# Kernel tuning notes

Hardware: AMD Instinct MI355X
Metric: run time of the kernel (lower is better)

## Reference

```python
import jax, jax.numpy as jnp
import numpy as np

D_MODEL = 512
OUT = 512
D_STATE = 16
D_CONV = 4
EXPAND = 2
N_LAYERS = 2
D_INNER = EXPAND * D_MODEL
DT_RANK = -(-D_MODEL // 16)  # ceil(d_model/16) = 32
B = 2
L = 2048


def setup_inputs() -> dict:
    key = jax.random.key(0)
    ks = jax.random.split(key, 16)
    def w(k, shape, scale):
        return jax.random.normal(k, shape, dtype=jnp.float32) * scale
    s_d = 1.0 / np.sqrt(D_MODEL)
    s_e = 1.0 / np.sqrt(D_INNER)
    s_r = 1.0 / np.sqrt(DT_RANK)
    s_f = 1.0 / np.sqrt(2 * D_MODEL)
    return {
        "x": jax.random.normal(ks[0], (B, L, D_MODEL), dtype=jnp.float32),
        "in_proj_w": w(ks[1], (N_LAYERS, 2 * D_INNER, D_MODEL), s_d),
        "conv_w": w(ks[2], (N_LAYERS, D_INNER, D_CONV), 0.5),
        "conv_b": jnp.zeros((N_LAYERS, D_INNER), jnp.float32),
        "x_proj_w": w(ks[3], (N_LAYERS, DT_RANK + 2 * D_STATE, D_INNER), s_e),
        "dt_w": w(ks[4], (N_LAYERS, D_INNER, DT_RANK), s_r),
        "dt_b": w(ks[5], (N_LAYERS, D_INNER), 0.1),
        "A_log": jnp.tile(jnp.log(jnp.arange(1, D_STATE + 1, dtype=jnp.float32))[None, None, :], (N_LAYERS, D_INNER, 1)),
        "Dp": jnp.ones((N_LAYERS, D_INNER), jnp.float32),
        "out_proj_w": w(ks[6], (N_LAYERS, D_MODEL, D_INNER), s_e),
        "rms_w": jnp.ones((N_LAYERS, D_MODEL), jnp.float32),
        "ln1_w": jnp.ones((D_MODEL,), jnp.float32),
        "ln1_b": jnp.zeros((D_MODEL,), jnp.float32),
        "ln2_w": jnp.ones((D_MODEL,), jnp.float32),
        "ln2_b": jnp.zeros((D_MODEL,), jnp.float32),
        "ffn_w1": w(ks[7], (2 * D_MODEL, D_MODEL), s_d),
        "ffn_b1": jnp.zeros((2 * D_MODEL,), jnp.float32),
        "ffn_w2": w(ks[8], (D_MODEL, 2 * D_MODEL), s_f),
        "ffn_b2": jnp.zeros((D_MODEL,), jnp.float32),
        "final_w": w(ks[9], (OUT, D_MODEL), s_d),
        "final_b": jnp.zeros((OUT,), jnp.float32),
    }


def _ln(x, w, b, eps=1e-5):
    mu = x.mean(-1, keepdims=True)
    v = ((x - mu) ** 2).mean(-1, keepdims=True)
    return (x - mu) * jax.lax.rsqrt(v + eps) * w + b


def _rms(x, w, eps=1e-5):
    return x * jax.lax.rsqrt(jnp.mean(x * x, -1, keepdims=True) + eps) * w


def _mixer(x, ipw, cw, cb, xpw, dtw, dtb, alog, dpar, opw):
    # x: [B, L, D]; single Mamba mixer (in_proj -> causal depthwise conv -> SSM -> gate -> out_proj)
    Lx = x.shape[1]
    xz = x @ ipw.T                              # [B, L, 2*ED]
    xc, z = jnp.split(xz, 2, axis=-1)
    xp = jnp.pad(xc, ((0, 0), (D_CONV - 1, 0), (0, 0)))  # causal left-pad
    xc = cb + sum(cw[:, k] * xp[:, k:k + Lx, :] for k in range(D_CONV))
    xc = jax.nn.silu(xc)
    dbc = xc @ xpw.T                            # [B, L, dt_rank + 2*N]
    delta = jax.nn.softplus(dbc[..., :DT_RANK] @ dtw.T + dtb)   # [B, L, ED]
    Bm = dbc[..., DT_RANK:DT_RANK + D_STATE]    # [B, L, N]
    Cm = dbc[..., DT_RANK + D_STATE:]           # [B, L, N]
    A = -jnp.exp(alog)                          # [ED, N]
    dA = jnp.exp(delta[..., None] * A)          # [B, L, ED, N]
    dBx = (delta * xc)[..., None] * Bm[:, :, None, :]  # [B, L, ED, N]
    def step(h, inp):
        a, bx = inp
        h = a * h + bx
        return h, h
    _, hs = jax.lax.scan(step, jnp.zeros_like(dA[:, 0]), (jnp.moveaxis(dA, 1, 0), jnp.moveaxis(dBx, 1, 0)))
    hs = jnp.moveaxis(hs, 0, 1)                 # [B, L, ED, N]
    y = jnp.einsum('blen,bln->ble', hs, Cm) + dpar * xc
    return (y * jax.nn.silu(z)) @ opw.T


def _forward(x, in_proj_w, conv_w, conv_b, x_proj_w, dt_w, dt_b, A_log, Dp, out_proj_w, rms_w,
             ln1_w, ln1_b, ln2_w, ln2_b, ffn_w1, ffn_b1, ffn_w2, ffn_b2, final_w, final_b):
    h = _ln(x, ln1_w, ln1_b)
    for i in range(N_LAYERS):  # Mamba = stack of residual RMSNorm+mixer blocks
        h = h + _mixer(_rms(h, rms_w[i]), in_proj_w[i], conv_w[i], conv_b[i], x_proj_w[i],
                       dt_w[i], dt_b[i], A_log[i], Dp[i], out_proj_w[i])
    x = x + h
    f = jax.nn.relu(_ln(x, ln2_w, ln2_b) @ ffn_w1.T + ffn_b1) @ ffn_w2.T + ffn_b2
    x = x + f
    return x @ final_w.T + final_b


def reference(x, in_proj_w, conv_w, conv_b, x_proj_w, dt_w, dt_b, A_log, Dp, out_proj_w, rms_w,
              ln1_w, ln1_b, ln2_w, ln2_b, ffn_w1, ffn_b1, ffn_w2, ffn_b2, final_w, final_b):
    return _forward(x, in_proj_w, conv_w, conv_b, x_proj_w, dt_w, dt_b, A_log, Dp, out_proj_w, rms_w,
                    ln1_w, ln1_b, ln2_w, ln2_b, ffn_w1, ffn_b1, ffn_w2, ffn_b2, final_w, final_b)
```

## Files before the change

### kernel.cpp

```cpp
#include <hip/hip_runtime.h>
#include <math.h>

#define ROWS 4096
#define LSEQ 2048
#define DM   512
#define DI   1024
#define NCH  64
#define CHT  (LSEQ / NCH)
#define NCOMB 1152

typedef __bf16 bf16_t;
typedef bf16_t bf16x8 __attribute__((ext_vector_type(8)));
typedef float f32x4 __attribute__((ext_vector_type(4)));
typedef unsigned int u32;
typedef const __attribute__((address_space(1))) u32* gp32;
typedef __attribute__((address_space(3))) u32* lp32;

__device__ __forceinline__ float siluf(float v) { return v / (1.f + expf(-v)); }
__device__ __forceinline__ float softplusf(float v) {
    return fmaxf(v, 0.f) + log1pf(expf(-fabsf(v)));
}

__global__ __launch_bounds__(256) void ln_kernel(const float* __restrict__ x,
                                                 const float* __restrict__ w,
                                                 const float* __restrict__ b,
                                                 float* __restrict__ out) {
    int row = blockIdx.x;
    int tid = threadIdx.x;
    const float* xr = x + (size_t)row * DM;
    float v0 = xr[tid], v1 = xr[tid + 256];
    float sum = v0 + v1, sq = v0 * v0 + v1 * v1;
    for (int o = 32; o > 0; o >>= 1) {
        sum += __shfl_down(sum, o);
        sq  += __shfl_down(sq, o);
    }
    __shared__ float s1[4], s2[4];
    int wid = tid >> 6, lane = tid & 63;
    if (lane == 0) { s1[wid] = sum; s2[wid] = sq; }
    __syncthreads();
    sum = s1[0] + s1[1] + s1[2] + s1[3];
    sq  = s2[0] + s2[1] + s2[2] + s2[3];
    float mu  = sum * (1.f / DM);
    float var = sq * (1.f / DM) - mu * mu;
    float r   = rsqrtf(var + 1e-5f);
    out[(size_t)row * DM + tid]       = (v0 - mu) * r * w[tid] + b[tid];
    out[(size_t)row * DM + tid + 256] = (v1 - mu) * r * w[tid + 256] + b[tid + 256];
}

__global__ __launch_bounds__(256) void ln_add_kernel(
    const float* __restrict__ x, const float* __restrict__ hres,
    const float* __restrict__ w, const float* __restrict__ b,
    float* __restrict__ x2, bf16_t* __restrict__ outb) {
    int row = blockIdx.x;
    int tid = threadIdx.x;
    size_t base = (size_t)row * DM;
    float v0 = x[base + tid] + hres[base + tid];
    float v1 = x[base + tid + 256] + hres[base + tid + 256];
    x2[base + tid] = v0;
    x2[base + tid + 256] = v1;
    float sum = v0 + v1, sq = v0 * v0 + v1 * v1;
    for (int o = 32; o > 0; o >>= 1) {
        sum += __shfl_down(sum, o);
        sq  += __shfl_down(sq, o);
    }
    __shared__ float s1[4], s2[4];
    int wid = tid >> 6, lane = tid & 63;
    if (lane == 0) { s1[wid] = sum; s2[wid] = sq; }
    __syncthreads();
    sum = s1[0] + s1[1] + s1[2] + s1[3];
    sq  = s2[0] + s2[1] + s2[2] + s2[3];
    float mu  = sum * (1.f / DM);
    float var = sq * (1.f / DM) - mu * mu;
    float r   = rsqrtf(var + 1e-5f);
    outb[base + tid]       = (bf16_t)((v0 - mu) * r * w[tid] + b[tid]);
    outb[base + tid + 256] = (bf16_t)((v1 - mu) * r * w[tid + 256] + b[tid + 256]);
}

__global__ __launch_bounds__(256) void rms_kernel(const float* __restrict__ x,
                                                  const float* __restrict__ w,
                                                  bf16_t* __restrict__ out) {
    int row = blockIdx.x;
    int tid = threadIdx.x;
    const float* xr = x + (size_t)row * DM;
    float v0 = xr[tid], v1 = xr[tid + 256];
    float sq = v0 * v0 + v1 * v1;
    for (int o = 32; o > 0; o >>= 1) sq += __shfl_down(sq, o);
    __shared__ float s2[4];
    int wid = tid >> 6, lane = tid & 63;
    if (lane == 0) s2[wid] = sq;
    __syncthreads();
    sq = s2[0] + s2[1] + s2[2] + s2[3];
    float r = rsqrtf(sq * (1.f / DM) + 1e-5f);
    out[(size_t)row * DM + tid]       = (bf16_t)(v0 * r * w[tid]);
    out[(size_t)row * DM + tid + 256] = (bf16_t)(v1 * r * w[tid + 256]);
}

__global__ __launch_bounds__(256) void cvt_kernel(
    const float* __restrict__ ipw, const float* __restrict__ opw,
    const float* __restrict__ fw1, const float* __restrict__ fw2,
    const float* __restrict__ finw, bf16_t* __restrict__ arena) {
    int idx = blockIdx.x * 256 + threadIdx.x;
    float v;
    if (idx < 2097152)      v = ipw[idx];
    else if (idx < 3145728) v = opw[idx - 2097152];
    else if (idx < 3670016) v = fw1[idx - 3145728];
    else if (idx < 4194304) v = fw2[idx - 3670016];
    else                    v = finw[idx - 4194304];
    arena[idx] = (bf16_t)v;
}

__global__ __launch_bounds__(256) void wd_kernel(
    const float* __restrict__ dtw, const float* __restrict__ xpw,
    bf16_t* __restrict__ wcomb) {
    int idx = blockIdx.x * 256 + threadIdx.x;
    int j = idx & 1023;
    int i = idx >> 10;
    float v;
    if (i < 1024) {
        const float* dr = dtw + i * 32;
        v = 0.f;
#pragma unroll
        for (int k = 0; k < 32; ++k) v = fmaf(dr[k], xpw[k * 1024 + j], v);
    } else if (i < 1056) {
        v = xpw[(i - 1024 + 32) * 1024 + j];
    } else {
        v = 0.f;
    }
    wcomb[idx] = (bf16_t)v;
}

template <int BMF, int ACT, bool BIAS, bool RES, bool OUTBF>
__global__ __launch_bounds__(256) void mgemm_kernel(
    const bf16_t* __restrict__ A, const bf16_t* __restrict__ W,
    const float* __restrict__ bias, const float* __restrict__ res,
    void* __restrict__ Cv, int nbn, int K, int ldc,
    const bf16_t* __restrict__ xcp, bf16_t* __restrict__ dxc,
    float* __restrict__ bcb, void* __restrict__ aux) {
    constexpr int BM = BMF * 32;
    __shared__ bf16_t As[BM * 64];
    __shared__ bf16_t Bs[128 * 64];
    const int tid  = threadIdx.x;
    const int lane = tid & 63;
    const int wave = tid >> 6;
    const int wr = wave >> 1, wc = wave & 1;
    const int l16 = lane & 15, kgrp = lane >> 4;
    const int prow = tid >> 3;
    const int pp   = tid & 7;
    const int wbase = (tid & ~63) * 8;
    const int cpx = (int)gridDim.x >> 3;
    const int id  = ((int)blockIdx.x & 7) * cpx + ((int)blockIdx.x >> 3);
    const int bn  = (id % nbn) * 128;
    const int bm  = (id / nbn) * BM;

    f32x4 acc[BMF][4] = {};

    for (int k0 = 0; k0 < K; k0 += 64) {
        __syncthreads();
#pragma unroll
        for (int it = 0; it < BMF; ++it) {
            int r  = it * 32 + prow;
            int gc = k0 + ((pp ^ (r & 7)) << 3);
            __builtin_amdgcn_global_load_lds(
                (gp32)(const void*)(A + (size_t)(bm + r) * K + gc),
                (lp32)(void*)(As + it * 2048 + wbase), 16, 0, 0);
        }
#pragma unroll
        for (int it = 0; it < 4; ++it) {
            int r  = it * 32 + prow;
            int gc = k0 + ((pp ^ (r & 7)) << 3);
            __builtin_amdgcn_global_load_lds(
                (gp32)(const void*)(W + (size_t)(bn + r) * K + gc),
                (lp32)(void*)(Bs + it * 2048 + wbase), 16, 0, 0);
        }
        __syncthreads();
#pragma unroll
        for (int ks = 0; ks < 2; ++ks) {
            bf16x8 af[BMF], bv[4];
#pragma unroll
            for (int i = 0; i < BMF; ++i) {
                int ra = wr * (BM / 2) + i * 16 + l16;
                af[i] = *(const bf16x8*)(As + ra * 64 + ((((ks << 2) | kgrp) ^ (ra & 7)) << 3));
            }
#pragma unroll
            for (int j = 0; j < 4; ++j) {
                int rb = wc * 64 + j * 16 + l16;
                bv[j] = *(const bf16x8*)(Bs + rb * 64 + ((((ks << 2) | kgrp) ^ (rb & 7)) << 3));
            }
#pragma unroll
            for (int i = 0; i < BMF; ++i)
#pragma unroll
                for (int j = 0; j < 4; ++j)
                    acc[i][j] = __builtin_amdgcn_mfma_f32_16x16x32_bf16(
                        af[i], bv[j], acc[i][j], 0, 0, 0);
        }
    }
#pragma unroll
    for (int i = 0; i < BMF; ++i) {
#pragma unroll
        for (int j = 0; j < 4; ++j) {
            int col = bn + wc * 64 + j * 16 + l16;
            if (ACT == 2) {
                if (col < 1024) {
                    float badd = bias[col];
#pragma unroll
                    for (int q = 0; q < 4; ++q) {
                        int row = bm + wr * (BM / 2) + i * 16 + kgrp * 4 + q;
                        float d = softplusf(acc[i][j][q] + badd);
                        ((bf16_t*)Cv)[(size_t)row * 1024 + col] = (bf16_t)d;
                        dxc[(size_t)row * 1024 + col] =
                            (bf16_t)(d * (float)xcp[(size_t)row * 1024 + col]);
                    }
                } else if (col < 1056) {
#pragma unroll
                    for (int q = 0; q < 4; ++q) {
                        int row = bm + wr * (BM / 2) + i * 16 + kgrp * 4 + q;
                        bcb[(size_t)row * 32 + (col - 1024)] = acc[i][j][q];
                    }
                }
            } else if (ACT == 3) {
#pragma unroll
                for (int q = 0; q < 4; ++q) {
                    int row = bm + wr * (BM / 2) + i * 16 + kgrp * 4 + q;
                    float v = acc[i][j][q];
                    if (col < 1024)
                        ((bf16_t*)Cv)[(size_t)row * 1024 + col] = (bf16_t)v;
                    else
                        ((bf16_t*)aux)[(size_t)row * 1024 + (col - 1024)] = (bf16_t)v;
                }
            } else {
                float badd = BIAS ? bias[col] : 0.f;
#pragma unroll
                for (int q = 0; q < 4; ++q) {
                    int row = bm + wr * (BM / 2) + i * 16 + kgrp * 4 + q;
                    float v = acc[i][j][q] + badd;
                    if (RES) v += res[(size_t)row * ldc + col];
                    if (ACT == 1) v = fmaxf(v, 0.f);
                    if (OUTBF) ((bf16_t*)Cv)[(size_t)row * ldc + col] = (bf16_t)v;
                    else       ((float*)Cv)[(size_t)row * ldc + col] = v;
                }
            }
        }
    }
}

__global__ __launch_bounds__(256) void conv_silu_kernel(
    const bf16_t* __restrict__ xraw, const float* __restrict__ cw,
    const float* __restrict__ cb, bf16_t* __restrict__ out) {
    int idx = blockIdx.x * blockDim.x + threadIdx.x;
    int c = idx & (DI - 1);
    int row = idx >> 10;
    int t = row & (LSEQ - 1);
    float acc = cb[c];
#pragma unroll
    for (int k = 0; k < 4; ++k) {
        int st = t + k - 3;
        if (st >= 0)
            acc = fmaf(cw[c * 4 + k], (float)xraw[(size_t)(row + k - 3) * 1024 + c], acc);
    }
    out[idx] = (bf16_t)siluf(acc);
}

__global__ __launch_bounds__(256) void scan1_kernel(
    const bf16_t* __restrict__ dbuf, const bf16_t* __restrict__ dxcb,
    const float* __restrict__ bc_in, const float* __restrict__ A_log,
    float* __restrict__ aprod, float* __restrict__ bacc) {
    int gid  = blockIdx.x * 256 + threadIdx.x;
    int e    = gid >> 1;
    int half = gid & 1;
    int ch = blockIdx.y;
    int b  = blockIdx.z;
    float cAn[8];
#pragma unroll
    for (int n = 0; n < 8; ++n)
        cAn[n] = -expf(A_log[e * 16 + half * 8 + n]) * 1.4426950408889634f;
    float ap[8], bc[8];
#pragma unroll
    for (int n = 0; n < 8; ++n) { ap[n] = 1.f; bc[n] = 0.f; }
    int row0 = b * LSEQ + ch * CHT;
    float d_c   = (float)dbuf[(size_t)row0 * DI + e];
    float dxc_c = (float)dxcb[(size_t)row0 * 1024 + e];
    for (int t = 0; t < CHT; ++t) {
        int row = row0 + t;
        float d_n = 0.f, dxc_n = 0.f;
        if (t + 1 < CHT) {
            d_n   = (float)dbuf[(size_t)(row + 1) * DI + e];
            dxc_n = (float)dxcb[(size_t)(row + 1) * 1024 + e];
        }
        const float* brow = bc_in + (size_t)row * 32 + half * 8;
        float4 b0 = *(const float4*)brow;
        float4 b1 = *(const float4*)(brow + 4);
        float Bn[8] = {b0.x, b0.y, b0.z, b0.w, b1.x, b1.y, b1.z, b1.w};
#pragma unroll
        for (int n = 0; n < 8; ++n) {
            float dA = exp2f(d_c * cAn[n]);
            ap[n] *= dA;
            bc[n] = fmaf(dA, bc[n], dxc_c * Bn[n]);
        }
        d_c = d_n; dxc_c = dxc_n;
    }
    size_t idx = ((size_t)((b * NCH + ch) * DI + e)) * 16 + half * 8;
    float4* apo = (float4*)(aprod + idx);
    float4* bco = (float4*)(bacc + idx);
#pragma unroll
    for (int q = 0; q < 2; ++q) {
        apo[q] = make_float4(ap[q * 4], ap[q * 4 + 1], ap[q * 4 + 2], ap[q * 4 + 3]);
        bco[q] = make_float4(bc[q * 4], bc[q * 4 + 1], bc[q * 4 + 2], bc[q * 4 + 3]);
    }
}

__global__ __launch_bounds__(256) void scan2a_kernel(
    const float* __restrict__ aprod, const float* __restrict__ bacc,
    float* __restrict__ gA, float* __restrict__ gB) {
    int t = blockIdx.x * 256 + threadIdx.x;
    int n = t & 15, e = (t >> 4) & 1023, grp = (t >> 14) & 7, b = t >> 17;
    float A = 1.f, B = 0.f;
    for (int i = 0; i < 8; ++i) {
        int ch = grp * 8 + i;
        size_t idx = ((size_t)((b * NCH + ch) * DI + e)) * 16 + n;
        float a = aprod[idx], bb = bacc[idx];
        A = a * A;
        B = fmaf(a, B, bb);
    }
    size_t g = ((size_t)((b * 8 + grp) * DI + e)) * 16 + n;
    gA[g] = A; gB[g] = B;
}
__global__ __launch_bounds__(256) void scan2b_kernel(
    const float* __restrict__ gA, const float* __restrict__ gB,
    float* __restrict__ ghin) {
    int t = blockIdx.x * 256 + threadIdx.x;
    int n = t & 15, e = (t >> 4) & 1023, b = t >> 14;
    float h = 0.f;
    for (int g = 0; g < 8; ++g) {
        size_t idx = ((size_t)((b * 8 + g) * DI + e)) * 16 + n;
        ghin[idx] = h;
        h = fmaf(gA[idx], h, gB[idx]);
    }
}
__global__ __launch_bounds__(256) void scan2c_kernel(
    const float* __restrict__ ghin, float* aprod_hinit,
    const float* __restrict__ bacc) {
    int t = blockIdx.x * 256 + threadIdx.x;
    int n = t & 15, e = (t >> 4) & 1023, grp = (t >> 14) & 7, b = t >> 17;
    float h = ghin[((size_t)((b * 8 + grp) * DI + e)) * 16 + n];
    for (int i = 0; i < 8; ++i) {
        int ch = grp * 8 + i;
        size_t idx = ((size_t)((b * NCH + ch) * DI + e)) * 16 + n;
        float a = aprod_hinit[idx], bb = bacc[idx];
        aprod_hinit[idx] = h;
        h = fmaf(a, h, bb);
    }
}

__global__ __launch_bounds__(256) void scan3_kernel(
    const bf16_t* __restrict__ dbuf, const bf16_t* __restrict__ dxcb,
    const bf16_t* __restrict__ xcb, const bf16_t* __restrict__ zb,
    const float* __restrict__ bc_in, const float* __restrict__ A_log,
    const float* __restrict__ Dp, const float* __restrict__ hinit,
    bf16_t* __restrict__ yg) {
    int gid  = blockIdx.x * 256 + threadIdx.x;
    int e    = gid >> 1;
    int half = gid & 1;
    int ch = blockIdx.y;
    int b  = blockIdx.z;
    float cAn[8];
#pragma unroll
    for (int n = 0; n < 8; ++n)
        cAn[n] = -expf(A_log[e * 16 + half * 8 + n]) * 1.4426950408889634f;
    float h[8];
    {
        const float4* hp = (const float4*)(hinit +
            ((size_t)((b * NCH + ch) * DI + e)) * 16 + half * 8);
#pragma unroll
        for (int q = 0; q < 2; ++q) {
            float4 v = hp[q];
            h[q * 4] = v.x; h[q * 4 + 1] = v.y; h[q * 4 + 2] = v.z; h[q * 4 + 3] = v.w;
        }
    }
    float Dpe = Dp[e];
    int row0 = b * LSEQ + ch * CHT;
    float d_c   = (float)dbuf[(size_t)row0 * DI + e];
    float dxc_c = (float)dxcb[(size_t)row0 * 1024 + e];
    float xc_c  = (float)xcb[(size_t)row0 * 1024 + e];
    float z_c   = (float)zb[(size_t)row0 * 1024 + e];
    for (int t = 0; t < CHT; ++t) {
        int row = row0 + t;
        float d_n = 0.f, dxc_n = 0.f, xc_n = 0.f, z_n = 0.f;
        if (t + 1 < CHT) {
            d_n   = (float)dbuf[(size_t)(row + 1) * DI + e];
            dxc_n = (float)dxcb[(size_t)(row + 1) * 1024 + e];
            xc_n  = (float)xcb[(size_t)(row + 1) * 1024 + e];
            z_n   = (float)zb[(size_t)(row + 1) * 1024 + e];
        }
        const float* brow = bc_in + (size_t)row * 32;
        float4 b0 = *(const float4*)(brow + half * 8);
        float4 b1 = *(const float4*)(brow + half * 8 + 4);
        float4 c0 = *(const float4*)(brow + 16 + half * 8);
        float4 c1 = *(const float4*)(brow + 16 + half * 8 + 4);
        float Bn[8] = {b0.x, b0.y, b0.z, b0.w, b1.x, b1.y, b1.z, b1.w};
        float Cn[8] = {c0.x, c0.y, c0.z, c0.w, c1.x, c1.y, c1.z, c1.w};
        float y = half ? 0.f : Dpe * xc_c;
#pragma unroll
        for (int n = 0; n < 8; ++n) {
            float dA = exp2f(d_c * cAn[n]);
            h[n] = fmaf(dA, h[n], dxc_c * Bn[n]);
            y = fmaf(h[n], Cn[n], y);
        }
        y += __shfl_xor(y, 1);
        if (half == 0)
            yg[(size_t)row * DI + e] = (bf16_t)(y * siluf(z_c));
        d_c = d_n; dxc_c = dxc_n; xc_c = xc_n; z_c = z_n;
    }
}

extern "C" void kernel_launch(void* const* d_in, const int* in_sizes, int n_in,
                              void* d_out, int out_size, void* d_ws, size_t ws_size,
                              hipStream_t stream) {
    const float* x    = (const float*)d_in[0];
    const float* ipw  = (const float*)d_in[1];
    const float* cw   = (const float*)d_in[2];
    const float* cb   = (const float*)d_in[3];
    const float* xpw  = (const float*)d_in[4];
    const float* dtw  = (const float*)d_in[5];
    const float* dtb  = (const float*)d_in[6];
    const float* alog = (const float*)d_in[7];
    const float* dpar = (const float*)d_in[8];
    const float* opw  = (const float*)d_in[9];
    const float* rmsw = (const float*)d_in[10];
    const float* ln1w = (const float*)d_in[11];
    const float* ln1b = (const float*)d_in[12];
    const float* ln2w = (const float*)d_in[13];
    const float* ln2b = (const float*)d_in[14];
    const float* fw1  = (const float*)d_in[15];
    const float* fb1  = (const float*)d_in[16];
    const float* fw2  = (const float*)d_in[17];
    const float* fb2  = (const float*)d_in[18];
    const float* finw = (const float*)d_in[19];
    const float* finb = (const float*)d_in[20];
    float* out = (float*)d_out;

    const size_t MF = 1u << 20;
    float*  ws     = (float*)d_ws;
    float*  h      = ws;
    bf16_t* hnb    = (bf16_t*)(ws + 2 * MF);
    bf16_t* xrawb  = (bf16_t*)(ws + 3 * MF);
    bf16_t* zb     = (bf16_t*)(ws + 5 * MF);
    bf16_t* xcb    = (bf16_t*)(ws + 7 * MF);
    bf16_t* dbufb  = (bf16_t*)(ws + 9 * MF);
    bf16_t* dxcbb  = (bf16_t*)(ws + 11 * MF);
    float*  bcbuf  = ws + 13 * MF;
    bf16_t* ygb    = (bf16_t*)(ws + 13 * MF + MF / 4);
    float*  aprod  = ws + 15 * MF + MF / 4;
    float*  bacc   = ws + 17 * MF + MF / 4;
    float*  gsA    = ws + 19 * MF + MF / 4;
    float*  gsB    = ws + 19 * MF + MF / 2;
    float*  ghin   = ws + 19 * MF + 3 * MF / 4;
    bf16_t* warena = (bf16_t*)(ws + 20 * MF);
    float*  x2     = (float*)dbufb;
    bf16_t* midb   = xcb;
    bf16_t* x3b    = dxcbb;
    float*  hinit  = aprod;
    const size_t IPW_OFF = 0, OPW_OFF = 2097152, FW1_OFF = 3145728,
                 FW2_OFF = 3670016, FINW_OFF = 4194304, WC_OFF = 4456448;

    cvt_kernel<<<17408, 256, 0, stream>>>(ipw, opw, fw1, fw2, finw, warena);
    for (int i = 0; i < 2; ++i)
        wd_kernel<<<NCOMB * 1024 / 256, 256, 0, stream>>>(
            dtw + (size_t)i * DI * 32, xpw + (size_t)i * 64 * DI,
            warena + WC_OFF + (size_t)i * NCOMB * 1024);
    ln_kernel<<<ROWS, 256, 0, stream>>>(x, ln1w, ln1b, h);

    for (int i = 0; i < 2; ++i) {
        const bf16_t* ipwb_i = warena + IPW_OFF + (size_t)i * 2048 * 512;
        const bf16_t* opwb_i = warena + OPW_OFF + (size_t)i * 512 * 1024;
        const bf16_t* wcombb = warena + WC_OFF + (size_t)i * NCOMB * 1024;
        const float* cw_i   = cw   + (size_t)i * DI * 4;
        const float* cb_i   = cb   + (size_t)i * DI;
        const float* dtb_i  = dtb  + (size_t)i * DI;
        const float* alog_i = alog + (size_t)i * DI * 16;
        const float* dp_i   = dpar + (size_t)i * DI;
        const float* rms_i  = rmsw + (size_t)i * DM;

        rms_kernel<<<ROWS, 256, 0, stream>>>(h, rms_i, hnb);
        mgemm_kernel<2, 3, false, false, false><<<1024, 256, 0, stream>>>(
            hnb, ipwb_i, nullptr, nullptr, xrawb, 16, 512, 1024,
            nullptr, nullptr, nullptr, zb);
        conv_silu_kernel<<<ROWS * DI / 256, 256, 0, stream>>>(xrawb, cw_i, cb_i, xcb);
        mgemm_kernel<2, 2, false, false, false><<<576, 256, 0, stream>>>(
            xcb, wcombb, dtb_i, nullptr, dbufb, 9, 1024, 1024,
            xcb, dxcbb, bcbuf, nullptr);
        scan1_kernel<<<dim3(8, NCH, 2), 256, 0, stream>>>(dbufb, dxcbb, bcbuf,
                                                          alog_i, aprod, bacc);
        scan2a_kernel<<<1024, 256, 0, stream>>>(aprod, bacc, gsA, gsB);
        scan2b_kernel<<<128, 256, 0, stream>>>(gsA, gsB, ghin);
        scan2c_kernel<<<1024, 256, 0, stream>>>(ghin, aprod, bacc);
        scan3_kernel<<<dim3(8, NCH, 2), 256, 0, stream>>>(dbufb, dxcbb, xcb, zb,
                                                          bcbuf, alog_i, dp_i,
                                                          hinit, ygb);
        mgemm_kernel<2, 0, false, true, false><<<256, 256, 0, stream>>>(
            ygb, opwb_i, nullptr, h, h, 4, 1024, DM,
            nullptr, nullptr, nullptr, nullptr);
    }

    ln_add_kernel<<<ROWS, 256, 0, stream>>>(x, h, ln2w, ln2b, x2, hnb);
    mgemm_kernel<2, 1, true, false, true><<<512, 256, 0, stream>>>(
        hnb, warena + FW1_OFF, fb1, nullptr, midb, 8, 512, DI,
        nullptr, nullptr, nullptr, nullptr);
    mgemm_kernel<2, 0, true, true, true><<<256, 256, 0, stream>>>(
        midb, warena + FW2_OFF, fb2, x2, x3b, 4, 1024, DM,
        nullptr, nullptr, nullptr, nullptr);
    mgemm_kernel<2, 0, true, false, false><<<256, 256, 0, stream>>>(
        x3b, warena + FINW_OFF, finb, nullptr, out, 4, 512, DM,
        nullptr, nullptr, nullptr, nullptr);
}
```

Baseline: 512.1 us.

## Double-buffer GEMM LDS tiles, drop dxc buffer, merge wd launches

The bf16 GEMM now uses two LDS buffers so the async global-to-LDS load of the next K tile is issued before the MFMAs on the current tile, with one barrier per iteration. The delta*xc product is no longer written by the dt GEMM epilogue; the scan kernels recompute it from d and xc, which removes one activation-sized write and its reads. The two per-layer wd_kernel launches are merged into one 2-D grid. Double buffering doubles LDS per block, which may reduce occupancy, and it relies on the trailing barrier to make the prefetched tile visible before it is read.

```diff
diff --git a/kernel.cpp b/kernel.cpp
--- a/kernel.cpp
+++ b/kernel.cpp
@@ -110,8 +110,12 @@
 }
 
 __global__ __launch_bounds__(256) void wd_kernel(
-    const float* __restrict__ dtw, const float* __restrict__ xpw,
-    bf16_t* __restrict__ wcomb) {
+    const float* __restrict__ dtw_all, const float* __restrict__ xpw_all,
+    bf16_t* __restrict__ wcomb_all) {
+    int layer = blockIdx.y;
+    const float* dtw = dtw_all + (size_t)layer * DI * 32;
+    const float* xpw = xpw_all + (size_t)layer * 64 * DI;
+    bf16_t* wcomb = wcomb_all + (size_t)layer * NCOMB * 1024;
     int idx = blockIdx.x * 256 + threadIdx.x;
     int j = idx & 1023;
     int i = idx >> 10;
@@ -134,11 +138,10 @@
     const bf16_t* __restrict__ A, const bf16_t* __restrict__ W,
     const float* __restrict__ bias, const float* __restrict__ res,
     void* __restrict__ Cv, int nbn, int K, int ldc,
-    const bf16_t* __restrict__ xcp, bf16_t* __restrict__ dxc,
     float* __restrict__ bcb, void* __restrict__ aux) {
     constexpr int BM = BMF * 32;
-    __shared__ bf16_t As[BM * 64];
-    __shared__ bf16_t Bs[128 * 64];
+    __shared__ bf16_t As[2][BM * 64];
+    __shared__ bf16_t Bs[2][128 * 64];
     const int tid  = threadIdx.x;
     const int lane = tid & 63;
     const int wave = tid >> 6;
@@ -154,37 +157,46 @@
 
     f32x4 acc[BMF][4] = {};
 
-    for (int k0 = 0; k0 < K; k0 += 64) {
-        __syncthreads();
-#pragma unroll
-        for (int it = 0; it < BMF; ++it) {
-            int r  = it * 32 + prow;
-            int gc = k0 + ((pp ^ (r & 7)) << 3);
-            __builtin_amdgcn_global_load_lds(
-                (gp32)(const void*)(A + (size_t)(bm + r) * K + gc),
-                (lp32)(void*)(As + it * 2048 + wbase), 16, 0, 0);
-        }
-#pragma unroll
-        for (int it = 0; it < 4; ++it) {
-            int r  = it * 32 + prow;
-            int gc = k0 + ((pp ^ (r & 7)) << 3);
-            __builtin_amdgcn_global_load_lds(
-                (gp32)(const void*)(W + (size_t)(bn + r) * K + gc),
-                (lp32)(void*)(Bs + it * 2048 + wbase), 16, 0, 0);
-        }
-        __syncthreads();
+#define STAGE(buf, k0)                                                        \
+    {                                                                         \
+        _Pragma("unroll")                                                     \
+        for (int it = 0; it < BMF; ++it) {                                    \
+            int r  = it * 32 + prow;                                          \
+            int gc = (k0) + ((pp ^ (r & 7)) << 3);                            \
+            __builtin_amdgcn_global_load_lds(                                 \
+                (gp32)(const void*)(A + (size_t)(bm + r) * K + gc),           \
+                (lp32)(void*)(As[buf] + it * 2048 + wbase), 16, 0, 0);        \
+        }                                                                     \
+        _Pragma("unroll")                                                     \
+        for (int it = 0; it < 4; ++it) {                                      \
+            int r  = it * 32 + prow;                                          \
+            int gc = (k0) + ((pp ^ (r & 7)) << 3);                            \
+            __builtin_amdgcn_global_load_lds(                                 \
+                (gp32)(const void*)(W + (size_t)(bn + r) * K + gc),           \
+                (lp32)(void*)(Bs[buf] + it * 2048 + wbase), 16, 0, 0);        \
+        }                                                                     \
+    }
+
+    const int NT = K >> 6;
+    STAGE(0, 0);
+    __syncthreads();
+    for (int t = 0; t < NT; ++t) {
+        const int cur = t & 1;
+        if (t + 1 < NT) STAGE(cur ^ 1, (t + 1) << 6);
 #pragma unroll
         for (int ks = 0; ks < 2; ++ks) {
             bf16x8 af[BMF], bv[4];
 #pragma unroll
             for (int i = 0; i < BMF; ++i) {
                 int ra = wr * (BM / 2) + i * 16 + l16;
-                af[i] = *(const bf16x8*)(As + ra * 64 + ((((ks << 2) | kgrp) ^ (ra & 7)) << 3));
+                af[i] = *(const bf16x8*)(As[cur] + ra * 64 +
+                        ((((ks << 2) | kgrp) ^ (ra & 7)) << 3));
             }
 #pragma unroll
             for (int j = 0; j < 4; ++j) {
                 int rb = wc * 64 + j * 16 + l16;
-                bv[j] = *(const bf16x8*)(Bs + rb * 64 + ((((ks << 2) | kgrp) ^ (rb & 7)) << 3));
+                bv[j] = *(const bf16x8*)(Bs[cur] + rb * 64 +
+                        ((((ks << 2) | kgrp) ^ (rb & 7)) << 3));
             }
 #pragma unroll
             for (int i = 0; i < BMF; ++i)
@@ -193,7 +205,9 @@
                     acc[i][j] = __builtin_amdgcn_mfma_f32_16x16x32_bf16(
                         af[i], bv[j], acc[i][j], 0, 0, 0);
         }
-    }
+        __syncthreads();
+    }
+#undef STAGE
 #pragma unroll
     for (int i = 0; i < BMF; ++i) {
 #pragma unroll
@@ -207,8 +221,6 @@
                         int row = bm + wr * (BM / 2) + i * 16 + kgrp * 4 + q;
                         float d = softplusf(acc[i][j][q] + badd);
                         ((bf16_t*)Cv)[(size_t)row * 1024 + col] = (bf16_t)d;
-                        dxc[(size_t)row * 1024 + col] =
-                            (bf16_t)(d * (float)xcp[(size_t)row * 1024 + col]);
                     }
                 } else if (col < 1056) {
 #pragma unroll
@@ -261,7 +273,7 @@
 }
 
 __global__ __launch_bounds__(256) void scan1_kernel(
-    const bf16_t* __restrict__ dbuf, const bf16_t* __restrict__ dxcb,
+    const bf16_t* __restrict__ dbuf, const bf16_t* __restrict__ xcb,
     const float* __restrict__ bc_in, const float* __restrict__ A_log,
     float* __restrict__ aprod, float* __restrict__ bacc) {
     int gid  = blockIdx.x * 256 + threadIdx.x;
@@ -277,26 +289,27 @@
 #pragma unroll
     for (int n = 0; n < 8; ++n) { ap[n] = 1.f; bc[n] = 0.f; }
     int row0 = b * LSEQ + ch * CHT;
-    float d_c   = (float)dbuf[(size_t)row0 * DI + e];
-    float dxc_c = (float)dxcb[(size_t)row0 * 1024 + e];
+    float d_c  = (float)dbuf[(size_t)row0 * DI + e];
+    float xc_c = (float)xcb[(size_t)row0 * 1024 + e];
     for (int t = 0; t < CHT; ++t) {
         int row = row0 + t;
-        float d_n = 0.f, dxc_n = 0.f;
+        float d_n = 0.f, xc_n = 0.f;
         if (t + 1 < CHT) {
-            d_n   = (float)dbuf[(size_t)(row + 1) * DI + e];
-            dxc_n = (float)dxcb[(size_t)(row + 1) * 1024 + e];
+            d_n  = (float)dbuf[(size_t)(row + 1) * DI + e];
+            xc_n = (float)xcb[(size_t)(row + 1) * 1024 + e];
         }
         const float* brow = bc_in + (size_t)row * 32 + half * 8;
         float4 b0 = *(const float4*)brow;
         float4 b1 = *(const float4*)(brow + 4);
         float Bn[8] = {b0.x, b0.y, b0.z, b0.w, b1.x, b1.y, b1.z, b1.w};
+        float dxc_c = d_c * xc_c;
 #pragma unroll
         for (int n = 0; n < 8; ++n) {
             float dA = exp2f(d_c * cAn[n]);
             ap[n] *= dA;
             bc[n] = fmaf(dA, bc[n], dxc_c * Bn[n]);
         }
-        d_c = d_n; dxc_c = dxc_n;
+        d_c = d_n; xc_c = xc_n;
     }
     size_t idx = ((size_t)((b * NCH + ch) * DI + e)) * 16 + half * 8;
     float4* apo = (float4*)(aprod + idx);
@@ -352,11 +365,10 @@
 }
 
 __global__ __launch_bounds__(256) void scan3_kernel(
-    const bf16_t* __restrict__ dbuf, const bf16_t* __restrict__ dxcb,
-    const bf16_t* __restrict__ xcb, const bf16_t* __restrict__ zb,
-    const float* __restrict__ bc_in, const float* __restrict__ A_log,
-    const float* __restrict__ Dp, const float* __restrict__ hinit,
-    bf16_t* __restrict__ yg) {
+    const bf16_t* __restrict__ dbuf, const bf16_t* __restrict__ xcb,
+    const bf16_t* __restrict__ zb, const float* __restrict__ bc_in,
+    const float* __restrict__ A_log, const float* __restrict__ Dp,
+    const float* __restrict__ hinit, bf16_t* __restrict__ yg) {
     int gid  = blockIdx.x * 256 + threadIdx.x;
     int e    = gid >> 1;
     int half = gid & 1;
@@ -378,18 +390,16 @@
     }
     float Dpe = Dp[e];
     int row0 = b * LSEQ + ch * CHT;
-    float d_c   = (float)dbuf[(size_t)row0 * DI + e];
-    float dxc_c = (float)dxcb[(size_t)row0 * 1024 + e];
-    float xc_c  = (float)xcb[(size_t)row0 * 1024 + e];
-    float z_c   = (float)zb[(size_t)row0 * 1024 + e];
+    float d_c  = (float)dbuf[(size_t)row0 * DI + e];
+    float xc_c = (float)xcb[(size_t)row0 * 1024 + e];
+    float z_c  = (float)zb[(size_t)row0 * 1024 + e];
     for (int t = 0; t < CHT; ++t) {
         int row = row0 + t;
-        float d_n = 0.f, dxc_n = 0.f, xc_n = 0.f, z_n = 0.f;
+        float d_n = 0.f, xc_n = 0.f, z_n = 0.f;
         if (t + 1 < CHT) {
-            d_n   = (float)dbuf[(size_t)(row + 1) * DI + e];
-            dxc_n = (float)dxcb[(size_t)(row + 1) * 1024 + e];
-            xc_n  = (float)xcb[(size_t)(row + 1) * 1024 + e];
-            z_n   = (float)zb[(size_t)(row + 1) * 1024 + e];
+            d_n  = (float)dbuf[(size_t)(row + 1) * DI + e];
+            xc_n = (float)xcb[(size_t)(row + 1) * 1024 + e];
+            z_n  = (float)zb[(size_t)(row + 1) * 1024 + e];
         }
         const float* brow = bc_in + (size_t)row * 32;
         float4 b0 = *(const float4*)(brow + half * 8);
@@ -398,6 +408,7 @@
         float4 c1 = *(const float4*)(brow + 16 + half * 8 + 4);
         float Bn[8] = {b0.x, b0.y, b0.z, b0.w, b1.x, b1.y, b1.z, b1.w};
         float Cn[8] = {c0.x, c0.y, c0.z, c0.w, c1.x, c1.y, c1.z, c1.w};
+        float dxc_c = d_c * xc_c;
         float y = half ? 0.f : Dpe * xc_c;
 #pragma unroll
         for (int n = 0; n < 8; ++n) {
@@ -408,7 +419,7 @@
         y += __shfl_xor(y, 1);
         if (half == 0)
             yg[(size_t)row * DI + e] = (bf16_t)(y * siluf(z_c));
-        d_c = d_n; dxc_c = dxc_n; xc_c = xc_n; z_c = z_n;
+        d_c = d_n; xc_c = xc_n; z_c = z_n;
     }
 }
 
@@ -446,7 +457,7 @@
     bf16_t* zb     = (bf16_t*)(ws + 5 * MF);
     bf16_t* xcb    = (bf16_t*)(ws + 7 * MF);
     bf16_t* dbufb  = (bf16_t*)(ws + 9 * MF);
-    bf16_t* dxcbb  = (bf16_t*)(ws + 11 * MF);
+    bf16_t* spareb = (bf16_t*)(ws + 11 * MF);
     float*  bcbuf  = ws + 13 * MF;
     bf16_t* ygb    = (bf16_t*)(ws + 13 * MF + MF / 4);
     float*  aprod  = ws + 15 * MF + MF / 4;
@@ -457,16 +468,14 @@
     bf16_t* warena = (bf16_t*)(ws + 20 * MF);
     float*  x2     = (float*)dbufb;
     bf16_t* midb   = xcb;
-    bf16_t* x3b    = dxcbb;
+    bf16_t* x3b    = spareb;
     float*  hinit  = aprod;
     const size_t IPW_OFF = 0, OPW_OFF = 2097152, FW1_OFF = 3145728,
                  FW2_OFF = 3670016, FINW_OFF = 4194304, WC_OFF = 4456448;
 
     cvt_kernel<<<17408, 256, 0, stream>>>(ipw, opw, fw1, fw2, finw, warena);
-    for (int i = 0; i < 2; ++i)
-        wd_kernel<<<NCOMB * 1024 / 256, 256, 0, stream>>>(
-            dtw + (size_t)i * DI * 32, xpw + (size_t)i * 64 * DI,
-            warena + WC_OFF + (size_t)i * NCOMB * 1024);
+    wd_kernel<<<dim3(NCOMB * 1024 / 256, 2), 256, 0, stream>>>(
+        dtw, xpw, warena + WC_OFF);
     ln_kernel<<<ROWS, 256, 0, stream>>>(x, ln1w, ln1b, h);
 
     for (int i = 0; i < 2; ++i) {
@@ -483,32 +492,32 @@
         rms_kernel<<<ROWS, 256, 0, stream>>>(h, rms_i, hnb);
         mgemm_kernel<2, 3, false, false, false><<<1024, 256, 0, stream>>>(
             hnb, ipwb_i, nullptr, nullptr, xrawb, 16, 512, 1024,
-            nullptr, nullptr, nullptr, zb);
+            nullptr, zb);
         conv_silu_kernel<<<ROWS * DI / 256, 256, 0, stream>>>(xrawb, cw_i, cb_i, xcb);
         mgemm_kernel<2, 2, false, false, false><<<576, 256, 0, stream>>>(
             xcb, wcombb, dtb_i, nullptr, dbufb, 9, 1024, 1024,
-            xcb, dxcbb, bcbuf, nullptr);
-        scan1_kernel<<<dim3(8, NCH, 2), 256, 0, stream>>>(dbufb, dxcbb, bcbuf,
+            bcbuf, nullptr);
+        scan1_kernel<<<dim3(8, NCH, 2), 256, 0, stream>>>(dbufb, xcb, bcbuf,
                                                           alog_i, aprod, bacc);
         scan2a_kernel<<<1024, 256, 0, stream>>>(aprod, bacc, gsA, gsB);
         scan2b_kernel<<<128, 256, 0, stream>>>(gsA, gsB, ghin);
         scan2c_kernel<<<1024, 256, 0, stream>>>(ghin, aprod, bacc);
-        scan3_kernel<<<dim3(8, NCH, 2), 256, 0, stream>>>(dbufb, dxcbb, xcb, zb,
+        scan3_kernel<<<dim3(8, NCH, 2), 256, 0, stream>>>(dbufb, xcb, zb,
                                                           bcbuf, alog_i, dp_i,
                                                           hinit, ygb);
         mgemm_kernel<2, 0, false, true, false><<<256, 256, 0, stream>>>(
             ygb, opwb_i, nullptr, h, h, 4, 1024, DM,
-            nullptr, nullptr, nullptr, nullptr);
+            nullptr, nullptr);
     }
 
     ln_add_kernel<<<ROWS, 256, 0, stream>>>(x, h, ln2w, ln2b, x2, hnb);
     mgemm_kernel<2, 1, true, false, true><<<512, 256, 0, stream>>>(
         hnb, warena + FW1_OFF, fb1, nullptr, midb, 8, 512, DI,
-        nullptr, nullptr, nullptr, nullptr);
+        nullptr, nullptr);
     mgemm_kernel<2, 0, true, true, true><<<256, 256, 0, stream>>>(
         midb, warena + FW2_OFF, fb2, x2, x3b, 4, 1024, DM,
-        nullptr, nullptr, nullptr, nullptr);
+        nullptr, nullptr);
     mgemm_kernel<2, 0, true, false, false><<<256, 256, 0, stream>>>(
         x3b, warena + FINW_OFF, finb, nullptr, out, 4, 512, DM,
-        nullptr, nullptr, nullptr, nullptr);
-}
+        nullptr, nullptr);
+}
```

After: 505.8 us. No clear change (-1.2%).
